# Optimization experiments

Measured on AMD Instinct MI355X. Metric: run time of the kernel, lower is better.

## Reference

```python
import jax, jax.numpy as jnp
import numpy as np

B, N, DIM = 2, 2048, 1024
HEADS, DIM_HEAD = 16, 64
INNER = HEADS * DIM_HEAD  # 1024
SCALE = DIM_HEAD ** -0.5


def setup_inputs() -> dict:
    key = jax.random.key(0)
    ks = jax.random.split(key, 6)
    s = lambda k, shape, fan: jax.random.normal(k, shape, jnp.float32) * (fan ** -0.5)
    return {
        "x": jax.random.normal(ks[0], (B, N, DIM), jnp.float32),
        "similarity": jax.random.normal(ks[1], (B, N), jnp.float32),
        "Wq": s(ks[2], (DIM, INNER), DIM),
        "Wkv": s(ks[3], (DIM, 2 * INNER), DIM),
        "Wo": s(ks[4], (INNER, DIM), INNER),
        "bo": jnp.zeros((DIM,), jnp.float32),
    }


def reference(x, similarity, Wq, Wkv, Wo, bo):
    b, n, _ = x.shape
    h, d = HEADS, DIM_HEAD
    # projections (context = x, self-attention)
    q = (x @ Wq).reshape(b, n, h, d).transpose(0, 2, 1, 3)        # b h n d
    kv = x @ Wkv                                                   # b n 2*inner
    k, v = jnp.split(kv, 2, axis=-1)
    k = k.reshape(b, n, h, d).transpose(0, 2, 1, 3)
    v = v.reshape(b, n, h, d).transpose(0, 2, 1, 3)
    dots = jnp.einsum('bhid,bhjd->bhij', q, k) * SCALE             # b h n n
    # similarity [b,n] -> broadcast as per-query row bias [b,1,n,1]
    dots = dots + similarity[:, None, :, None]
    attn = jax.nn.softmax(dots, axis=-1)
    out = jnp.einsum('bhij,bhjd->bhid', attn, v)                   # b h n d
    out = out.transpose(0, 2, 1, 3).reshape(b, n, h * d)           # b n inner
    return out @ Wo + bo
```

## Files before the change

kernel.cpp:

```cpp
#include <hip/hip_runtime.h>


typedef __attribute__((ext_vector_type(8))) short short8;
typedef __attribute__((ext_vector_type(4))) float float4_;
typedef __attribute__((ext_vector_type(16))) float floatx16;
typedef __attribute__((ext_vector_type(4))) unsigned short ushort4_;
typedef __attribute__((ext_vector_type(4))) unsigned int uint4_;

#define MFMA(a, b, c) __builtin_amdgcn_mfma_f32_16x16x32_bf16((a), (b), (c), 0, 0, 0)
#define MFMA32(a, b, c) __builtin_amdgcn_mfma_f32_32x32x16_bf16((a), (b), (c), 0, 0, 0)

static __device__ __forceinline__ unsigned short f2bf(float f) {
    union { float f; unsigned int u; } v; v.f = f;
    unsigned int r = v.u + 0x7FFFu + ((v.u >> 16) & 1u);
    return (unsigned short)(r >> 16);
}

static __device__ __forceinline__ void gld16(const void* g, void* l) {
    __builtin_amdgcn_global_load_lds(
        (__attribute__((address_space(1))) void*)(g),
        (__attribute__((address_space(3))) void*)(l), 16, 0, 0);
}

__global__ __launch_bounds__(256) void prep(
    const float* __restrict__ X, const float* __restrict__ Wq,
    const float* __restrict__ Wkv, const float* __restrict__ Wo,
    unsigned short* __restrict__ xb, unsigned short* __restrict__ Wt,
    unsigned short* __restrict__ Wot)
{
    const int bid = blockIdx.x, t = threadIdx.x;
    if (bid >= 1024) {
        const int b = bid - 1024;
        const float4_* src = (const float4_*)X;
        ushort4_* dst = (ushort4_*)xb;
        #pragma unroll
        for (int g = 0; g < 8; ++g) {
            const int idx = b * 2048 + g * 256 + t;
            float4_ v = src[idx];
            ushort4_ o;
            o[0] = f2bf(v[0]); o[1] = f2bf(v[1]);
            o[2] = f2bf(v[2]); o[3] = f2bf(v[3]);
            dst[idx] = o;
        }
        return;
    }
    __shared__ float tile[64][65];
    const float* src; unsigned short* dst; int N, kt, nt, drow0;
    if (bid < 256)      { src = Wq;  N = 1024; kt = bid & 15;       nt = bid >> 4;       dst = Wt;  drow0 = nt * 64; }
    else if (bid < 768) { src = Wkv; N = 2048; kt = (bid-256) & 15; nt = (bid-256) >> 4; dst = Wt;  drow0 = 1024 + nt * 64; }
    else                { src = Wo;  N = 1024; kt = (bid-768) & 15; nt = (bid-768) >> 4; dst = Wot; drow0 = nt * 64; }
    const int k0 = kt * 64, n0 = nt * 64;
    const int r0 = t >> 6, c = t & 63;
    #pragma unroll
    for (int i = 0; i < 16; ++i) {
        const int r = i * 4 + r0;
        tile[r][c] = src[(size_t)(k0 + r) * N + n0 + c];
    }
    __syncthreads();
    #pragma unroll
    for (int i = 0; i < 16; ++i) {
        const int rn = i * 4 + r0;
        dst[(size_t)(drow0 + rn) * 1024 + k0 + c] = f2bf(tile[c][rn]);
    }
}

__global__ __launch_bounds__(256) void qkv_gemm2(
    const unsigned short* __restrict__ xb, const unsigned short* __restrict__ Wt,
    unsigned short* __restrict__ q_ws, unsigned short* __restrict__ k_ws,
    unsigned short* __restrict__ vt_ws)
{
    __shared__ unsigned short As[128 * 64];
    __shared__ unsigned short Bs[128 * 64];
    const int t = threadIdx.x, wave = t >> 6, lane = t & 63;
    const int L = lane & 15, quad = lane >> 4;
    const int xcd = blockIdx.x & 7, idx = blockIdx.x >> 3;
    const int mb = (xcd >> 1) * 8 + (idx & 7);
    const int nb = (xcd & 1) * 12 + (idx >> 3);
    const int m0 = mb * 128, n0 = nb * 128;
    const int wr = wave >> 1, wc = wave & 1;

    float4_ z = {0.f, 0.f, 0.f, 0.f};
    float4_ acc[4][4];
    #pragma unroll
    for (int i = 0; i < 4; ++i)
        #pragma unroll
        for (int j = 0; j < 4; ++j) acc[i][j] = z;

    const unsigned short* gA[4]; const unsigned short* gB[4];
    unsigned short* lA[4]; unsigned short* lB[4];
    #pragma unroll
    for (int j = 0; j < 4; ++j) {
        const int cid = wave * 256 + j * 64 + lane;
        const int row = cid >> 3, pc = cid & 7;
        const int lch = pc ^ (row & 7);
        gA[j] = xb + (size_t)(m0 + row) * 1024 + lch * 8;
        gB[j] = Wt + (size_t)(n0 + row) * 1024 + lch * 8;
        lA[j] = As + wave * 2048 + j * 512;
        lB[j] = Bs + wave * 2048 + j * 512;
    }

    for (int kc = 0; kc < 1024; kc += 64) {
        #pragma unroll
        for (int j = 0; j < 4; ++j) {
            gld16(gA[j] + kc, lA[j]);
            gld16(gB[j] + kc, lB[j]);
        }
        __syncthreads();
        #pragma unroll
        for (int ks = 0; ks < 2; ++ks) {
            short8 af[4], bfr[4];
            #pragma unroll
            for (int mt = 0; mt < 4; ++mt) {
                const int rl = wr * 64 + mt * 16 + L;
                af[mt] = *(const short8*)(As + rl * 64 + (((ks * 4 + quad) ^ (L & 7)) << 3));
            }
            #pragma unroll
            for (int nt = 0; nt < 4; ++nt) {
                const int rl = wc * 64 + nt * 16 + L;
                bfr[nt] = *(const short8*)(Bs + rl * 64 + (((ks * 4 + quad) ^ (L & 7)) << 3));
            }
            #pragma unroll
            for (int mt = 0; mt < 4; ++mt)
                #pragma unroll
                for (int nt = 0; nt < 4; ++nt)
                    acc[mt][nt] = MFMA(af[mt], bfr[nt], acc[mt][nt]);
        }
        __syncthreads();
    }

    const int b = m0 >> 11;
    const int type = n0 >> 10;
    #pragma unroll
    for (int mt = 0; mt < 4; ++mt) {
        const int m = (m0 & 2047) + wr * 64 + mt * 16 + quad * 4;
        #pragma unroll
        for (int nt = 0; nt < 4; ++nt) {
            const int cl = (n0 & 1023) + wc * 64 + nt * 16 + L;
            const int h = cl >> 6, d = cl & 63;
            float4_ v = acc[mt][nt];
            if (type == 0) {
                unsigned short* p = q_ws + ((size_t)(b * 16 + h) * 2048 + m) * 64 + d;
                #pragma unroll
                for (int r = 0; r < 4; ++r) p[(size_t)r * 64] = f2bf(v[r] * 0.18033688011f);
            } else if (type == 1) {
                unsigned short* p = k_ws + ((size_t)(b * 16 + h) * 2048 + m) * 64 + d;
                #pragma unroll
                for (int r = 0; r < 4; ++r) p[(size_t)r * 64] = f2bf(v[r]);
            } else {
                ushort4_ pk;
                pk[0] = f2bf(v[0]); pk[1] = f2bf(v[1]);
                pk[2] = f2bf(v[2]); pk[3] = f2bf(v[3]);
                *(ushort4_*)(vt_ws + ((size_t)(b * 16 + h) * 64 + d) * 2048 + m) = pk;
            }
        }
    }
}

__global__ __launch_bounds__(256) void attn_fwd5(
    const unsigned short* __restrict__ q_ws,
    const unsigned short* __restrict__ k_ws,
    const unsigned short* __restrict__ vt_ws,
    unsigned short* __restrict__ o2)
{
    __shared__ unsigned short k_lds[2][64 * 64];
    __shared__ unsigned short v_lds[2][64 * 64];
    __shared__ float ls[4][32];
    const int t = threadIdx.x, wave = t >> 6, lane = t & 63;
    const int l32 = lane & 31, hi = lane >> 5;
    const int xcd = blockIdx.x & 7, loc = blockIdx.x >> 3;
    const int bh = xcd * 4 + (loc >> 4);
    const int qb = loc & 15;

    const unsigned short* Kp = k_ws + (size_t)bh * 2048 * 64;
    const unsigned short* Vt = vt_ws + (size_t)bh * 64 * 2048;

    const unsigned short* Qp = q_ws + ((size_t)bh * 2048 + qb * 128 + wave * 32 + l32) * 64;
    short8 qf[4];
    #pragma unroll
    for (int k = 0; k < 4; ++k) qf[k] = *(const short8*)(Qp + hi * 8 + k * 16);

    const int c0 = wave * 64 + lane;
    const int kr0 = c0 >> 3, kl0 = (c0 & 7) ^ (kr0 & 7);
    const int pr0 = (kr0 & ~12) | ((kr0 & 4) << 1) | ((kr0 & 8) >> 1);
    const unsigned short* ks0 = Kp + (size_t)pr0 * 64 + kl0 * 8;
    const unsigned short* ks1 = ks0 + 32 * 64;
    const unsigned short* vs0 = Vt + (size_t)kr0 * 2048 + kl0 * 8;
    const unsigned short* vs1 = Vt + (size_t)(kr0 + 32) * 2048 + kl0 * 8;
    const int dst0 = wave * 512, dst1 = 2048 + wave * 512;

    floatx16 o0, o1;
    #pragma unroll
    for (int r = 0; r < 16; ++r) { o0[r] = 0.f; o1[r] = 0.f; }
    float lsum = 0.f;

    gld16(ks0, k_lds[0] + dst0); gld16(ks1, k_lds[0] + dst1);
    gld16(vs0, v_lds[0] + dst0); gld16(vs1, v_lds[0] + dst1);
    __syncthreads();

    const int sw = l32 & 7;
    #pragma unroll 2
    for (int it = 0; it < 32; ++it) {
        const int p = it & 1;
        if (it + 1 < 32) {
            const int np = p ^ 1;
            const int joff = (it + 1) * 64;
            gld16(ks0 + (size_t)joff * 64, k_lds[np] + dst0);
            gld16(ks1 + (size_t)joff * 64, k_lds[np] + dst1);
            gld16(vs0 + joff, v_lds[np] + dst0);
            gld16(vs1 + joff, v_lds[np] + dst1);
        }
        const unsigned short* kb = k_lds[p];
        const unsigned short* vb = v_lds[p];

        floatx16 s0, s1;
        #pragma unroll
        for (int r = 0; r < 16; ++r) { s0[r] = 0.f; s1[r] = 0.f; }
        #pragma unroll
        for (int k = 0; k < 4; ++k) {
            const int lch = 2 * k + hi;
            short8 k0 = *(const short8*)(kb + l32 * 64 + ((lch ^ sw) << 3));
            short8 k1 = *(const short8*)(kb + (32 + l32) * 64 + ((lch ^ sw) << 3));
            s0 = MFMA32(k0, qf[k], s0);
            s1 = MFMA32(k1, qf[k], s1);
        }

        unsigned int pk0[8], pk1[8];
        #pragma unroll
        for (int d = 0; d < 8; ++d) {
            union { float f; unsigned int u; } a0, b0, a1, b1;
            a0.f = __builtin_amdgcn_exp2f(s0[2 * d]);
            b0.f = __builtin_amdgcn_exp2f(s0[2 * d + 1]);
            a1.f = __builtin_amdgcn_exp2f(s1[2 * d]);
            b1.f = __builtin_amdgcn_exp2f(s1[2 * d + 1]);
            lsum += (a0.f + b0.f) + (a1.f + b1.f);
            pk0[d] = __builtin_amdgcn_perm(b0.u, a0.u, 0x07060302u);
            pk1[d] = __builtin_amdgcn_perm(b1.u, a1.u, 0x07060302u);
        }

        #pragma unroll
        for (int w = 0; w < 4; ++w) {
            uint4_ pw;
            if (w == 0)      { pw[0] = pk0[0]; pw[1] = pk0[1]; pw[2] = pk0[2]; pw[3] = pk0[3]; }
            else if (w == 1) { pw[0] = pk0[4]; pw[1] = pk0[5]; pw[2] = pk0[6]; pw[3] = pk0[7]; }
            else if (w == 2) { pw[0] = pk1[0]; pw[1] = pk1[1]; pw[2] = pk1[2]; pw[3] = pk1[3]; }
            else             { pw[0] = pk1[4]; pw[1] = pk1[5]; pw[2] = pk1[6]; pw[3] = pk1[7]; }
            short8 pa = *(short8*)&pw;
            const int c = 2 * w + hi;
            short8 vf0 = *(const short8*)(vb + l32 * 64 + ((c ^ sw) << 3));
            short8 vf1 = *(const short8*)(vb + (32 + l32) * 64 + ((c ^ sw) << 3));
            o0 = MFMA32(pa, vf0, o0);
            o1 = MFMA32(pa, vf1, o1);
        }
        __syncthreads();
    }

    float ltot = lsum + __shfl_xor(lsum, 32);
    ls[wave][l32] = ltot;
    float inv[16];
    #pragma unroll
    for (int r = 0; r < 16; ++r)
        inv[r] = 1.0f / ls[wave][(r & 3) + 8 * (r >> 2) + 4 * hi];

    const int b = bh >> 4, h = bh & 15;
    unsigned short* ob = o2 + ((size_t)b * 2048 + qb * 128 + wave * 32) * 1024 + h * 64;
    #pragma unroll
    for (int r = 0; r < 16; ++r) {
        const int row = (r & 3) + 8 * (r >> 2) + 4 * hi;
        ob[(size_t)row * 1024 + l32]      = f2bf(o0[r] * inv[r]);
        ob[(size_t)row * 1024 + 32 + l32] = f2bf(o1[r] * inv[r]);
    }
}

__global__ __launch_bounds__(256) void out_gemm2(
    const unsigned short* __restrict__ o2, const unsigned short* __restrict__ Wot,
    const float* __restrict__ bo, float* __restrict__ Out)
{
    __shared__ unsigned short As[128 * 64];
    __shared__ unsigned short Bs[64 * 64];
    const int t = threadIdx.x, wave = t >> 6, lane = t & 63;
    const int L = lane & 15, quad = lane >> 4;
    const int xcd = blockIdx.x & 7, idx = blockIdx.x >> 3;
    const int mb = (xcd >> 1) * 8 + (idx & 7);
    const int nb = (xcd & 1) * 8 + (idx >> 3);
    const int m0 = mb * 128, n0 = nb * 64;
    const int wr = wave >> 1, wc = wave & 1;

    float4_ z = {0.f, 0.f, 0.f, 0.f};
    float4_ acc[4][2];
    #pragma unroll
    for (int i = 0; i < 4; ++i)
        #pragma unroll
        for (int j = 0; j < 2; ++j) acc[i][j] = z;

    const unsigned short* gA[4]; unsigned short* lA[4];
    #pragma unroll
    for (int j = 0; j < 4; ++j) {
        const int cid = wave * 256 + j * 64 + lane;
        const int row = cid >> 3, pc = cid & 7;
        gA[j] = o2 + (size_t)(m0 + row) * 1024 + (pc ^ (row & 7)) * 8;
        lA[j] = As + wave * 2048 + j * 512;
    }
    const unsigned short* gB[2]; unsigned short* lB[2];
    #pragma unroll
    for (int j = 0; j < 2; ++j) {
        const int cid = wave * 128 + j * 64 + lane;
        const int row = cid >> 3, pc = cid & 7;
        gB[j] = Wot + (size_t)(n0 + row) * 1024 + (pc ^ (row & 7)) * 8;
        lB[j] = Bs + wave * 1024 + j * 512;
    }

    for (int kc = 0; kc < 1024; kc += 64) {
        #pragma unroll
        for (int j = 0; j < 4; ++j) gld16(gA[j] + kc, lA[j]);
        #pragma unroll
        for (int j = 0; j < 2; ++j) gld16(gB[j] + kc, lB[j]);
        __syncthreads();
        #pragma unroll
        for (int ks = 0; ks < 2; ++ks) {
            short8 af[4], bfr[2];
            #pragma unroll
            for (int mt = 0; mt < 4; ++mt) {
                const int rl = wr * 64 + mt * 16 + L;
                af[mt] = *(const short8*)(As + rl * 64 + (((ks * 4 + quad) ^ (L & 7)) << 3));
            }
            #pragma unroll
            for (int nt = 0; nt < 2; ++nt) {
                const int rl = wc * 32 + nt * 16 + L;
                bfr[nt] = *(const short8*)(Bs + rl * 64 + (((ks * 4 + quad) ^ (L & 7)) << 3));
            }
            #pragma unroll
            for (int mt = 0; mt < 4; ++mt)
                #pragma unroll
                for (int nt = 0; nt < 2; ++nt)
                    acc[mt][nt] = MFMA(af[mt], bfr[nt], acc[mt][nt]);
        }
        __syncthreads();
    }

    #pragma unroll
    for (int mt = 0; mt < 4; ++mt) {
        const int m = m0 + wr * 64 + mt * 16 + quad * 4;
        #pragma unroll
        for (int nt = 0; nt < 2; ++nt) {
            const int c = n0 + wc * 32 + nt * 16 + L;
            const float bias = bo[c];
            #pragma unroll
            for (int r = 0; r < 4; ++r)
                Out[(size_t)(m + r) * 1024 + c] = acc[mt][nt][r] + bias;
        }
    }
}

extern "C" void kernel_launch(void* const* d_in, const int* in_sizes, int n_in,
                              void* d_out, int out_size, void* d_ws, size_t ws_size,
                              hipStream_t stream) {
    const float* x   = (const float*)d_in[0];
    const float* Wq  = (const float*)d_in[2];
    const float* Wkv = (const float*)d_in[3];
    const float* Wo  = (const float*)d_in[4];
    const float* bo  = (const float*)d_in[5];
    float* out = (float*)d_out;

    char* ws = (char*)d_ws;
    const size_t MB = 1024 * 1024;
    unsigned short* xb   = (unsigned short*)(ws);
    unsigned short* o2   = xb;
    unsigned short* Wt   = (unsigned short*)(ws + 8 * MB);
    unsigned short* Wot  = (unsigned short*)(ws + 14 * MB);
    unsigned short* q_ws = (unsigned short*)(ws + 16 * MB);
    unsigned short* k_ws = (unsigned short*)(ws + 24 * MB);
    unsigned short* vt_ws= (unsigned short*)(ws + 32 * MB);

    prep<<<dim3(1536), dim3(256), 0, stream>>>(x, Wq, Wkv, Wo, xb, Wt, Wot);
    qkv_gemm2<<<dim3(768), dim3(256), 0, stream>>>(xb, Wt, q_ws, k_ws, vt_ws);
    attn_fwd5<<<dim3(512), dim3(256), 0, stream>>>(q_ws, k_ws, vt_ws, o2);
    out_gemm2<<<dim3(512), dim3(256), 0, stream>>>(o2, Wot, bo, out);
}
```

Baseline: 185.1 us.

## Restructure attention to stream K/V from registers with split-KV waves

```diff
diff --git a/kernel.cpp b/kernel.cpp
--- a/kernel.cpp
+++ b/kernel.cpp
@@ -143,131 +143,145 @@
                 #pragma unroll
                 for (int r = 0; r < 4; ++r) p[(size_t)r * 64] = f2bf(v[r] * 0.18033688011f);
             } else if (type == 1) {
-                unsigned short* p = k_ws + ((size_t)(b * 16 + h) * 2048 + m) * 64 + d;
+                unsigned short* p = k_ws + (size_t)(b * 16 + h) * 131072
+                    + (m >> 5) * 2048 + (d >> 3) * 256 + (m & 31) * 8 + (d & 7);
                 #pragma unroll
-                for (int r = 0; r < 4; ++r) p[(size_t)r * 64] = f2bf(v[r]);
+                for (int r = 0; r < 4; ++r) p[r * 8] = f2bf(v[r]);
             } else {
                 ushort4_ pk;
                 pk[0] = f2bf(v[0]); pk[1] = f2bf(v[1]);
                 pk[2] = f2bf(v[2]); pk[3] = f2bf(v[3]);
-                *(ushort4_*)(vt_ws + ((size_t)(b * 16 + h) * 64 + d) * 2048 + m) = pk;
-            }
-        }
-    }
-}
-
-__global__ __launch_bounds__(256) void attn_fwd5(
+                *(ushort4_*)(vt_ws + (size_t)(b * 16 + h) * 131072
+                    + (m >> 3) * 512 + d * 8 + (m & 7)) = pk;
+            }
+        }
+    }
+}
+
+#define LOADT(k0_, k1_, k2_, k3_, v00_, v10_, v01_, v11_, IT) do {            \
+    const unsigned short* kp_ = kbase + (IT) * 2048;                          \
+    const unsigned short* vp_ = vbase + (IT) * 2048;                          \
+    k0_ = *(const short8*)(kp_);        k1_ = *(const short8*)(kp_ + 512);    \
+    k2_ = *(const short8*)(kp_ + 1024); k3_ = *(const short8*)(kp_ + 1536);   \
+    v00_ = *(const short8*)(vp_);        v10_ = *(const short8*)(vp_ + 1024); \
+    v01_ = *(const short8*)(vp_ + 256);  v11_ = *(const short8*)(vp_ + 1280); \
+} while (0)
+
+#define COMPT(k0_, k1_, k2_, k3_, v00_, v10_, v01_, v11_) do {                \
+    _Pragma("unroll")                                                         \
+    for (int qt = 0; qt < 4; ++qt) {                                          \
+        floatx16 s;                                                           \
+        _Pragma("unroll")                                                     \
+        for (int r = 0; r < 16; ++r) s[r] = 0.f;                              \
+        s = MFMA32(k0_, qf[qt][0], s);                                        \
+        s = MFMA32(k1_, qf[qt][1], s);                                        \
+        s = MFMA32(k2_, qf[qt][2], s);                                        \
+        s = MFMA32(k3_, qf[qt][3], s);                                        \
+        unsigned int pk[8];                                                   \
+        _Pragma("unroll")                                                     \
+        for (int d = 0; d < 8; ++d) {                                         \
+            union { float f; unsigned int u; } a_, b_;                        \
+            a_.f = __builtin_amdgcn_exp2f(s[2 * d]);                          \
+            b_.f = __builtin_amdgcn_exp2f(s[2 * d + 1]);                      \
+            pk[d] = __builtin_amdgcn_perm(b_.u, a_.u, 0x07060302u);           \
+        }                                                                     \
+        uint4_ w0_, w1_;                                                      \
+        w0_[0] = pk[0]; w0_[1] = pk[1]; w0_[2] = pk[2]; w0_[3] = pk[3];       \
+        w1_[0] = pk[4]; w1_[1] = pk[5]; w1_[2] = pk[6]; w1_[3] = pk[7];       \
+        short8 pa0 = *(short8*)&w0_, pa1 = *(short8*)&w1_;                    \
+        lac[qt] = MFMA32(pa0, ONES, lac[qt]);                                 \
+        lac[qt] = MFMA32(pa1, ONES, lac[qt]);                                 \
+        o[qt][0] = MFMA32(pa0, v00_, o[qt][0]);                               \
+        o[qt][0] = MFMA32(pa1, v10_, o[qt][0]);                               \
+        o[qt][1] = MFMA32(pa0, v01_, o[qt][1]);                               \
+        o[qt][1] = MFMA32(pa1, v11_, o[qt][1]);                               \
+    }                                                                         \
+} while (0)
+
+__global__ __launch_bounds__(128, 1) void attn_fwd6(
     const unsigned short* __restrict__ q_ws,
     const unsigned short* __restrict__ k_ws,
     const unsigned short* __restrict__ vt_ws,
     unsigned short* __restrict__ o2)
 {
-    __shared__ unsigned short k_lds[2][64 * 64];
-    __shared__ unsigned short v_lds[2][64 * 64];
-    __shared__ float ls[4][32];
+    __shared__ float cb[2][6144];
     const int t = threadIdx.x, wave = t >> 6, lane = t & 63;
     const int l32 = lane & 31, hi = lane >> 5;
     const int xcd = blockIdx.x & 7, loc = blockIdx.x >> 3;
     const int bh = xcd * 4 + (loc >> 4);
     const int qb = loc & 15;
 
-    const unsigned short* Kp = k_ws + (size_t)bh * 2048 * 64;
-    const unsigned short* Vt = vt_ws + (size_t)bh * 64 * 2048;
-
-    const unsigned short* Qp = q_ws + ((size_t)bh * 2048 + qb * 128 + wave * 32 + l32) * 64;
-    short8 qf[4];
-    #pragma unroll
-    for (int k = 0; k < 4; ++k) qf[k] = *(const short8*)(Qp + hi * 8 + k * 16);
-
-    const int c0 = wave * 64 + lane;
-    const int kr0 = c0 >> 3, kl0 = (c0 & 7) ^ (kr0 & 7);
-    const int pr0 = (kr0 & ~12) | ((kr0 & 4) << 1) | ((kr0 & 8) >> 1);
-    const unsigned short* ks0 = Kp + (size_t)pr0 * 64 + kl0 * 8;
-    const unsigned short* ks1 = ks0 + 32 * 64;
-    const unsigned short* vs0 = Vt + (size_t)kr0 * 2048 + kl0 * 8;
-    const unsigned short* vs1 = Vt + (size_t)(kr0 + 32) * 2048 + kl0 * 8;
-    const int dst0 = wave * 512, dst1 = 2048 + wave * 512;
-
-    floatx16 o0, o1;
-    #pragma unroll
-    for (int r = 0; r < 16; ++r) { o0[r] = 0.f; o1[r] = 0.f; }
-    float lsum = 0.f;
-
-    gld16(ks0, k_lds[0] + dst0); gld16(ks1, k_lds[0] + dst1);
-    gld16(vs0, v_lds[0] + dst0); gld16(vs1, v_lds[0] + dst1);
+    short8 qf[4][4];
+    #pragma unroll
+    for (int qt = 0; qt < 4; ++qt) {
+        const unsigned short* Qp = q_ws
+            + ((size_t)(bh * 2048 + qb * 128 + qt * 32 + l32)) * 64 + hi * 8;
+        #pragma unroll
+        for (int ks = 0; ks < 4; ++ks)
+            qf[qt][ks] = *(const short8*)(Qp + ks * 16);
+    }
+
+    const int piRow = (l32 & ~12) | ((l32 & 4) << 1) | ((l32 & 8) >> 1);
+    const unsigned short* kbase = k_ws + (size_t)bh * 131072
+        + wave * 65536 + hi * 256 + piRow * 8;
+    const unsigned short* vbase = vt_ws + (size_t)bh * 131072
+        + wave * 65536 + hi * 512 + l32 * 8;
+
+    short8 ONES;
+    #pragma unroll
+    for (int i = 0; i < 8; ++i) ONES[i] = (short)0x3F80;
+
+    floatx16 o[4][2], lac[4];
+    #pragma unroll
+    for (int qt = 0; qt < 4; ++qt) {
+        #pragma unroll
+        for (int r = 0; r < 16; ++r) {
+            o[qt][0][r] = 0.f; o[qt][1][r] = 0.f; lac[qt][r] = 0.f;
+        }
+    }
+
+    short8 kA0, kA1, kA2, kA3, vA00, vA10, vA01, vA11;
+    short8 kB0, kB1, kB2, kB3, vB00, vB10, vB01, vB11;
+    LOADT(kA0, kA1, kA2, kA3, vA00, vA10, vA01, vA11, 0);
+
+    #pragma unroll 1
+    for (int it = 0; it < 32; it += 2) {
+        LOADT(kB0, kB1, kB2, kB3, vB00, vB10, vB01, vB11, it + 1);
+        COMPT(kA0, kA1, kA2, kA3, vA00, vA10, vA01, vA11);
+        LOADT(kA0, kA1, kA2, kA3, vA00, vA10, vA01, vA11, (it + 2) & 31);
+        COMPT(kB0, kB1, kB2, kB3, vB00, vB10, vB01, vB11);
+    }
+
+    float* myb = cb[wave];
+    const int don = wave ? 0 : 2;
+    #pragma unroll
+    for (int g = 0; g < 2; ++g) {
+        const int qt = don + g;
+        #pragma unroll
+        for (int r = 0; r < 16; ++r) {
+            myb[(g * 48 + r)      * 64 + lane] = o[qt][0][r];
+            myb[(g * 48 + 16 + r) * 64 + lane] = o[qt][1][r];
+            myb[(g * 48 + 32 + r) * 64 + lane] = lac[qt][r];
+        }
+    }
     __syncthreads();
-
-    const int sw = l32 & 7;
-    #pragma unroll 2
-    for (int it = 0; it < 32; ++it) {
-        const int p = it & 1;
-        if (it + 1 < 32) {
-            const int np = p ^ 1;
-            const int joff = (it + 1) * 64;
-            gld16(ks0 + (size_t)joff * 64, k_lds[np] + dst0);
-            gld16(ks1 + (size_t)joff * 64, k_lds[np] + dst1);
-            gld16(vs0 + joff, v_lds[np] + dst0);
-            gld16(vs1 + joff, v_lds[np] + dst1);
-        }
-        const unsigned short* kb = k_lds[p];
-        const unsigned short* vb = v_lds[p];
-
-        floatx16 s0, s1;
-        #pragma unroll
-        for (int r = 0; r < 16; ++r) { s0[r] = 0.f; s1[r] = 0.f; }
-        #pragma unroll
-        for (int k = 0; k < 4; ++k) {
-            const int lch = 2 * k + hi;
-            short8 k0 = *(const short8*)(kb + l32 * 64 + ((lch ^ sw) << 3));
-            short8 k1 = *(const short8*)(kb + (32 + l32) * 64 + ((lch ^ sw) << 3));
-            s0 = MFMA32(k0, qf[k], s0);
-            s1 = MFMA32(k1, qf[k], s1);
-        }
-
-        unsigned int pk0[8], pk1[8];
-        #pragma unroll
-        for (int d = 0; d < 8; ++d) {
-            union { float f; unsigned int u; } a0, b0, a1, b1;
-            a0.f = __builtin_amdgcn_exp2f(s0[2 * d]);
-            b0.f = __builtin_amdgcn_exp2f(s0[2 * d + 1]);
-            a1.f = __builtin_amdgcn_exp2f(s1[2 * d]);
-            b1.f = __builtin_amdgcn_exp2f(s1[2 * d + 1]);
-            lsum += (a0.f + b0.f) + (a1.f + b1.f);
-            pk0[d] = __builtin_amdgcn_perm(b0.u, a0.u, 0x07060302u);
-            pk1[d] = __builtin_amdgcn_perm(b1.u, a1.u, 0x07060302u);
-        }
-
-        #pragma unroll
-        for (int w = 0; w < 4; ++w) {
-            uint4_ pw;
-            if (w == 0)      { pw[0] = pk0[0]; pw[1] = pk0[1]; pw[2] = pk0[2]; pw[3] = pk0[3]; }
-            else if (w == 1) { pw[0] = pk0[4]; pw[1] = pk0[5]; pw[2] = pk0[6]; pw[3] = pk0[7]; }
-            else if (w == 2) { pw[0] = pk1[0]; pw[1] = pk1[1]; pw[2] = pk1[2]; pw[3] = pk1[3]; }
-            else             { pw[0] = pk1[4]; pw[1] = pk1[5]; pw[2] = pk1[6]; pw[3] = pk1[7]; }
-            short8 pa = *(short8*)&pw;
-            const int c = 2 * w + hi;
-            short8 vf0 = *(const short8*)(vb + l32 * 64 + ((c ^ sw) << 3));
-            short8 vf1 = *(const short8*)(vb + (32 + l32) * 64 + ((c ^ sw) << 3));
-            o0 = MFMA32(pa, vf0, o0);
-            o1 = MFMA32(pa, vf1, o1);
-        }
-        __syncthreads();
-    }
-
-    float ltot = lsum + __shfl_xor(lsum, 32);
-    ls[wave][l32] = ltot;
-    float inv[16];
-    #pragma unroll
-    for (int r = 0; r < 16; ++r)
-        inv[r] = 1.0f / ls[wave][(r & 3) + 8 * (r >> 2) + 4 * hi];
-
+    const float* otb = cb[wave ^ 1];
+    const int own = wave ? 2 : 0;
     const int b = bh >> 4, h = bh & 15;
-    unsigned short* ob = o2 + ((size_t)b * 2048 + qb * 128 + wave * 32) * 1024 + h * 64;
-    #pragma unroll
-    for (int r = 0; r < 16; ++r) {
-        const int row = (r & 3) + 8 * (r >> 2) + 4 * hi;
-        ob[(size_t)row * 1024 + l32]      = f2bf(o0[r] * inv[r]);
-        ob[(size_t)row * 1024 + 32 + l32] = f2bf(o1[r] * inv[r]);
+    unsigned short* obase = o2 + ((size_t)(b * 2048 + qb * 128)) * 1024 + h * 64;
+    #pragma unroll
+    for (int g = 0; g < 2; ++g) {
+        const int qt = own + g;
+        #pragma unroll
+        for (int r = 0; r < 16; ++r) {
+            const float o0v = o[qt][0][r] + otb[(g * 48 + r)      * 64 + lane];
+            const float o1v = o[qt][1][r] + otb[(g * 48 + 16 + r) * 64 + lane];
+            const float lv  = lac[qt][r]  + otb[(g * 48 + 32 + r) * 64 + lane];
+            const float iv = 1.0f / lv;
+            const int row = qt * 32 + (r & 3) + 8 * (r >> 2) + 4 * hi;
+            obase[(size_t)row * 1024 + l32]      = f2bf(o0v * iv);
+            obase[(size_t)row * 1024 + 32 + l32] = f2bf(o1v * iv);
+        }
     }
 }
 
@@ -373,6 +387,6 @@
 
     prep<<<dim3(1536), dim3(256), 0, stream>>>(x, Wq, Wkv, Wo, xb, Wt, Wot);
     qkv_gemm2<<<dim3(768), dim3(256), 0, stream>>>(xb, Wt, q_ws, k_ws, vt_ws);
-    attn_fwd5<<<dim3(512), dim3(256), 0, stream>>>(q_ws, k_ws, vt_ws, o2);
+    attn_fwd6<<<dim3(512), dim3(128), 0, stream>>>(q_ws, k_ws, vt_ws, o2);
     out_gemm2<<<dim3(512), dim3(256), 0, stream>>>(o2, Wot, bo, out);
 }
```

New measurement: 203.2 us. 1.1x slower.
